# Kernel optimization log

Measured on AMD Instinct MI355X. Metric: run time of the kernel, lower is better.

Reference implementation:

```python
import jax, jax.numpy as jnp
import numpy as np

HEADS = 12
DIM = 768


def setup_inputs() -> dict:
    key = jax.random.key(0)
    ks = jax.random.split(key, 4)
    s = 0.02
    return {
        "x": jax.random.normal(ks[0], (8, 64, 64, DIM), dtype=jnp.float32),
        "w_qkv_h": jax.random.normal(ks[1], (DIM, 3 * DIM), dtype=jnp.float32) * s,
        "b_qkv_h": jnp.zeros((3 * DIM,), jnp.float32),
        "w_qkv_w": jax.random.normal(ks[2], (DIM, 3 * DIM), dtype=jnp.float32) * s,
        "b_qkv_w": jnp.zeros((3 * DIM,), jnp.float32),
        "w_proj": jax.random.normal(ks[3], (DIM, DIM), dtype=jnp.float32) * s,
        "b_proj": jnp.zeros((DIM,), jnp.float32),
    }


def _axial_attn(x_seq, w, b, heads, scale):
    # x_seq: [N, L, C]. Faithful to original torch code: q,k,v keep shape
    # [N, L, heads, hd]; matmul contracts hd, producing [N, L, heads, heads]
    # attention ACROSS HEADS at each position (no head permute in the source).
    N, L, C = x_seq.shape
    hd = C // heads
    qkv = (x_seq @ w + b).reshape(N, L, 3, heads, hd)
    q = qkv[:, :, 0] * scale
    k = qkv[:, :, 1]
    v = qkv[:, :, 2]
    attn = jax.nn.softmax(jnp.einsum('nlhd,nlgd->nlhg', q, k), axis=-1)
    out = jnp.einsum('nlhg,nlgd->nlhd', attn, v)
    return out.reshape(N, L, C)


def reference(x, w_qkv_h, b_qkv_h, w_qkv_w, b_qkv_w, w_proj, b_proj):
    B, H, W, C = x.shape
    scale = (C // HEADS) ** -0.5
    # H-axis pass: permute to [B, W, H, C], flatten batch*W
    x_h = jnp.transpose(x, (0, 2, 1, 3)).reshape(B * W, H, C)
    out_h = _axial_attn(x_h, w_qkv_h, b_qkv_h, HEADS, scale)
    out_h = jnp.transpose(out_h.reshape(B, W, H, C), (0, 2, 1, 3))
    # W-axis pass: flatten batch*H
    out_w = _axial_attn(x.reshape(B * H, W, C), w_qkv_w, b_qkv_w, HEADS, scale)
    out_w = out_w.reshape(B, H, W, C)
    # residual-style sum of the two axes, then output projection (dropout p=0)
    return (out_h + out_w) @ w_proj + b_proj
```

## Files before the change

kernel.cpp:

```cpp
#include <hip/hip_runtime.h>

typedef unsigned short u16;
typedef unsigned int u32;
typedef __attribute__((ext_vector_type(8))) short short8;
typedef __attribute__((ext_vector_type(4))) float f32x4;

#define DIMC 768
#define NQKV 2304
#define NPOS 32768
#define NKT 12

__device__ __forceinline__ float b2f(u16 u) {
    union { u32 i; float f; } c; c.i = ((u32)u) << 16; return c.f;
}
__device__ __forceinline__ u16 f2b(float f) {
    union { float f; u32 i; } c; c.f = f;
    u32 r = c.i + 0x7fffu + ((c.i >> 16) & 1u);
    return (u16)(r >> 16);
}

__device__ __forceinline__ void gl_lds16(const void* g, void* l) {
    __builtin_amdgcn_global_load_lds(
        (const __attribute__((address_space(1))) void*)g,
        (__attribute__((address_space(3))) void*)l, 16, 0, 0);
}

__global__ __launch_bounds__(256) void cvt_bf16(
    const float* __restrict__ in, u16* __restrict__ out, int n4)
{
    int i = blockIdx.x * 256 + threadIdx.x;
    if (i >= n4) return;
    float4 v = ((const float4*)in)[i];
    ushort4 o;
    o.x = f2b(v.x); o.y = f2b(v.y); o.z = f2b(v.z); o.w = f2b(v.w);
    ((ushort4*)out)[i] = o;
}

__global__ __launch_bounds__(256) void cvt_wT(
    const float* __restrict__ W0, const float* __restrict__ W1,
    const float* __restrict__ W2,
    u16* __restrict__ T0, u16* __restrict__ T1, u16* __restrict__ T2)
{
    const int z = blockIdx.z;
    const float* W = (z == 0) ? W0 : (z == 1) ? W1 : W2;
    u16* WT = (z == 0) ? T0 : (z == 1) ? T1 : T2;
    const int N = (z == 2) ? 768 : 2304;
    const int nb = blockIdx.x, kb = blockIdx.y;
    if (nb * 64 >= N) return;
    __shared__ u16 T[64][65];
    const int t = threadIdx.x, sr = t >> 2, sc = t & 3;
    {
        const float4* p = (const float4*)(W + (size_t)(kb * 64 + sr) * N + nb * 64 + sc * 16);
        float4 a0 = p[0], a1 = p[1], a2 = p[2], a3 = p[3];
        float vv[16] = {a0.x, a0.y, a0.z, a0.w, a1.x, a1.y, a1.z, a1.w,
                        a2.x, a2.y, a2.z, a2.w, a3.x, a3.y, a3.z, a3.w};
        #pragma unroll
        for (int i = 0; i < 16; ++i)
            T[sc * 16 + i][sr] = f2b(vv[i]);
    }
    __syncthreads();
    {
        u16 vv[16];
        #pragma unroll
        for (int i = 0; i < 16; ++i) vv[i] = T[sr][sc * 16 + i];
        uint4 p0, p1;
        p0.x = vv[0] | ((u32)vv[1] << 16);  p0.y = vv[2] | ((u32)vv[3] << 16);
        p0.z = vv[4] | ((u32)vv[5] << 16);  p0.w = vv[6] | ((u32)vv[7] << 16);
        p1.x = vv[8] | ((u32)vv[9] << 16);  p1.y = vv[10] | ((u32)vv[11] << 16);
        p1.z = vv[12] | ((u32)vv[13] << 16); p1.w = vv[14] | ((u32)vv[15] << 16);
        u16* q = WT + (size_t)(nb * 64 + sr) * DIMC + kb * 64 + sc * 16;
        *(uint4*)q = p0;
        *(uint4*)(q + 8) = p1;
    }
}


#define STAGE_A(buf, kt, ht) do {                                              \
    gl_lds16(aS + (size_t)((ht) * 128)      * DIMC + (size_t)(kt) * 64,        \
             &As[buf][(ht) * 8192 +        w * 512]);                          \
    gl_lds16(aS + (size_t)((ht) * 128 + 64) * DIMC + (size_t)(kt) * 64,        \
             &As[buf][(ht) * 8192 + 4096 + w * 512]);                          \
} while (0)

#define STAGE_B(buf, kt, ht) do {                                              \
    gl_lds16(bS + (size_t)((ht) * 128)      * DIMC + (size_t)(kt) * 64,        \
             &Bs[buf][(ht) * 8192 +        w * 512]);                          \
    gl_lds16(bS + (size_t)((ht) * 128 + 64) * DIMC + (size_t)(kt) * 64,        \
             &Bs[buf][(ht) * 8192 + 4096 + w * 512]);                          \
} while (0)

#define READ_A(base, hm) do {                                                  \
    _Pragma("unroll")                                                          \
    for (int i_ = 0; i_ < 4; ++i_) {                                           \
        const int row_ = (hm) * 128 + wm * 64 + i_ * 16 + lr;                  \
        _Pragma("unroll")                                                      \
        for (int ks_ = 0; ks_ < 2; ++ks_)                                      \
            af[i_][ks_] = *(const short8*)((base) + (row_ << 6) +              \
                              (((ks_ * 4 + lq) ^ (row_ & 7)) << 3));           \
    }                                                                          \
} while (0)

#define READ_B(dst, base, hn) do {                                             \
    _Pragma("unroll")                                                          \
    for (int j_ = 0; j_ < 2; ++j_) {                                           \
        const int row_ = (hn) * 128 + wn * 32 + j_ * 16 + lr;                  \
        _Pragma("unroll")                                                      \
        for (int ks_ = 0; ks_ < 2; ++ks_)                                      \
            (dst)[j_][ks_] = *(const short8*)((base) + (row_ << 6) +           \
                              (((ks_ * 4 + lq) ^ (row_ & 7)) << 3));           \
    }                                                                          \
} while (0)

#define MM(hm, hn, bsrc) do {                                                  \
    __builtin_amdgcn_s_setprio(1);                                             \
    _Pragma("unroll")                                                          \
    for (int i_ = 0; i_ < 4; ++i_)                                             \
        _Pragma("unroll")                                                      \
        for (int j_ = 0; j_ < 2; ++j_)                                         \
            _Pragma("unroll")                                                  \
            for (int ks_ = 0; ks_ < 2; ++ks_)                                  \
                acc[(hm) * 4 + i_][(hn) * 2 + j_] =                            \
                    __builtin_amdgcn_mfma_f32_16x16x32_bf16(                   \
                        af[i_][ks_], (bsrc)[j_][ks_],                          \
                        acc[(hm) * 4 + i_][(hn) * 2 + j_], 0, 0, 0);           \
    __builtin_amdgcn_s_setprio(0);                                             \
} while (0)

#define BAR() do {                                                             \
    __builtin_amdgcn_sched_barrier(0);                                         \
    __builtin_amdgcn_s_barrier();                                              \
    __builtin_amdgcn_sched_barrier(0);                                         \
} while (0)

#define KTILE(kt, S12, S34, VN) do {                                           \
    const int p_ = (kt) & 1, q_ = p_ ^ 1;                                      \
    const u16* Ab_ = As[p_];                                                   \
    const u16* Bb_ = Bs[p_];                                                   \
                                                             \
    READ_A(Ab_, 0);                                                            \
    READ_B(b0, Bb_, 0);                                                        \
    if (S12) STAGE_B(q_, (kt) + 1, 1);                                         \
    BAR();                                                                     \
    MM(0, 0, b0);                                                              \
                                                             \
    READ_B(b1, Bb_, 1);                                                        \
    if (S12) STAGE_A(q_, (kt) + 1, 1);                                         \
    BAR();                                                                     \
    MM(0, 1, b1);                                                              \
                                                             \
    READ_A(Ab_, 1);                                                            \
    if (S34) STAGE_A(p_, (kt) + 2, 0);                                         \
    BAR();                                                                     \
    MM(1, 0, b0);                                                              \
                                                             \
    if (S34) STAGE_B(p_, (kt) + 2, 0);                                         \
    __builtin_amdgcn_sched_barrier(0);                                         \
    asm volatile("s_waitcnt vmcnt(" VN ")" ::: "memory");                      \
    BAR();                                                                     \
    MM(1, 1, b1);                                                              \
} while (0)

__global__ __launch_bounds__(512, 2) void gemm256(
    const u16* __restrict__ A, const u16* __restrict__ BT,
    const float* __restrict__ bias, void* __restrict__ C,
    int ldn, int c_is_f32)
{
    __shared__ __align__(16) u16 As[2][256 * 64];
    __shared__ __align__(16) u16 Bs[2][256 * 64];

    const int t = threadIdx.x;
    const int w = t >> 6, l = t & 63;
    const int wm = w >> 2, wn = w & 3;
    const int lr = l & 15, lq = l >> 4;

    const int gx = (int)gridDim.x;
    const int nwg = gx * (int)gridDim.y;
    const int lin = (int)blockIdx.y * gx + (int)blockIdx.x;
    const int swz = (lin & 7) * (nwg >> 3) + (lin >> 3);
    const int by = swz / gx, bx = swz - by * gx;
    const int mBase = by * 256, nBase = bx * 256;

    const int srow = t >> 3;
    const int schk = (t & 7) ^ (srow & 7);
    const u16* aS = A  + (size_t)(mBase + srow) * DIMC + schk * 8;
    const u16* bS = BT + (size_t)(nBase + srow) * DIMC + schk * 8;

    f32x4 acc[8][4];
    #pragma unroll
    for (int i = 0; i < 8; ++i)
        #pragma unroll
        for (int j = 0; j < 4; ++j)
            acc[i][j] = (f32x4){0.f, 0.f, 0.f, 0.f};

    short8 af[4][2], b0[2][2], b1[2][2];

    STAGE_A(0, 0, 0); STAGE_B(0, 0, 0); STAGE_B(0, 0, 1); STAGE_A(0, 0, 1);
    STAGE_A(1, 1, 0); STAGE_B(1, 1, 0);
    __builtin_amdgcn_sched_barrier(0);
    asm volatile("s_waitcnt vmcnt(4)" ::: "memory");
    BAR();

    #pragma unroll 1
    for (int kt = 0; kt < NKT - 2; ++kt) { KTILE(kt, 1, 1, "4"); }
    { KTILE(NKT - 2, 1, 0, "0"); }
    { KTILE(NKT - 1, 0, 0, "0"); }

    #pragma unroll
    for (int hn = 0; hn < 2; ++hn)
        #pragma unroll
        for (int j = 0; j < 2; ++j) {
            const int col = nBase + hn * 128 + wn * 32 + j * 16 + lr;
            const float bb = bias[col];
            #pragma unroll
            for (int hm = 0; hm < 2; ++hm)
                #pragma unroll
                for (int i = 0; i < 4; ++i) {
                    const int row = mBase + hm * 128 + wm * 64 + i * 16 + lq * 4;
                    #pragma unroll
                    for (int rg = 0; rg < 4; ++rg) {
                        float v = acc[hm * 4 + i][hn * 2 + j][rg] + bb;
                        size_t idx = (size_t)(row + rg) * ldn + col;
                        if (c_is_f32) ((float*)C)[idx] = v;
                        else          ((u16*)C)[idx]   = f2b(v);
                    }
                }
        }
}

__device__ __forceinline__ void attn_one(
    short8 qa0, short8 qa1, short8 kb0, short8 kb1,
    const float* v, float* o, int lr)
{
    f32x4 s = (f32x4){0.f, 0.f, 0.f, 0.f};
    s = __builtin_amdgcn_mfma_f32_16x16x32_bf16(qa0, kb0, s, 0, 0, 0);
    s = __builtin_amdgcn_mfma_f32_16x16x32_bf16(qa1, kb1, s, 0, 0, 0);
    float pp[4];
    #pragma unroll
    for (int rg = 0; rg < 4; ++rg) {
        float x = (lr < 12) ? s[rg] * 0.125f : -1e30f;
        float m = x;
        m = fmaxf(m, __shfl_xor(m, 1));
        m = fmaxf(m, __shfl_xor(m, 2));
        m = fmaxf(m, __shfl_xor(m, 4));
        m = fmaxf(m, __shfl_xor(m, 8));
        float e = (lr < 12) ? __expf(x - m) : 0.f;
        float ss = e;
        ss += __shfl_xor(ss, 1);
        ss += __shfl_xor(ss, 2);
        ss += __shfl_xor(ss, 4);
        ss += __shfl_xor(ss, 8);
        pp[rg] = e / ss;
    }
    #pragma unroll
    for (int g = 0; g < 12; ++g) {
        #pragma unroll
        for (int h = 0; h < 12; ++h) {
            union { float f; int i; } cb;
            cb.i = __builtin_amdgcn_readlane(
                __builtin_bit_cast(int, pp[h & 3]), (h >> 2) * 16 + g);
            o[h] = fmaf(cb.f, v[g], o[h]);
        }
    }
}

__global__ __launch_bounds__(256) void headattn2(
    const u16* __restrict__ qkv1, const u16* __restrict__ qkv2,
    u16* __restrict__ sum)
{
    const int t = threadIdx.x, wv = t >> 6, l = t & 63;
    const int p = blockIdx.x * 4 + wv;
    const u16* r1 = qkv1 + (size_t)p * NQKV;
    const u16* r2 = qkv2 + (size_t)p * NQKV;
    const int lr = l & 15;
    const int fo = lr * 64 + (l >> 4) * 8;

    short8 qa0_1 = *(const short8*)(r1 + fo);
    short8 qa1_1 = *(const short8*)(r1 + fo + 32);
    short8 kb0_1 = *(const short8*)(r1 + 768 + fo);
    short8 kb1_1 = *(const short8*)(r1 + 768 + fo + 32);
    short8 qa0_2 = *(const short8*)(r2 + fo);
    short8 qa1_2 = *(const short8*)(r2 + fo + 32);
    short8 kb0_2 = *(const short8*)(r2 + 768 + fo);
    short8 kb1_2 = *(const short8*)(r2 + 768 + fo + 32);
    float v1[12], v2[12];
    #pragma unroll
    for (int g = 0; g < 12; ++g) {
        v1[g] = b2f(r1[1536 + g * 64 + l]);
        v2[g] = b2f(r2[1536 + g * 64 + l]);
    }

    float o[12];
    #pragma unroll
    for (int h = 0; h < 12; ++h) o[h] = 0.f;

    attn_one(qa0_1, qa1_1, kb0_1, kb1_1, v1, o, lr);
    attn_one(qa0_2, qa1_2, kb0_2, kb1_2, v2, o, lr);

    u16* orow = sum + (size_t)p * DIMC;
    #pragma unroll
    for (int h = 0; h < 12; ++h)
        orow[h * 64 + l] = f2b(o[h]);
}

extern "C" void kernel_launch(void* const* d_in, const int* in_sizes, int n_in,
                              void* d_out, int out_size, void* d_ws, size_t ws_size,
                              hipStream_t stream) {
    const float* x  = (const float*)d_in[0];
    const float* wh = (const float*)d_in[1];
    const float* bh = (const float*)d_in[2];
    const float* ww = (const float*)d_in[3];
    const float* bw = (const float*)d_in[4];
    const float* wp = (const float*)d_in[5];
    const float* bp = (const float*)d_in[6];
    float* out = (float*)d_out;

    u16* xb   = (u16*)d_ws;
    u16* sumb = xb;
    u16* whT  = xb   + 25165824;
    u16* wwT  = whT  + 1769472;
    u16* wpT  = wwT  + 1769472;
    u16* qkv1 = wpT  + 589824;
    u16* qkv2 = qkv1 + 75497472;

    cvt_bf16<<<24576, 256, 0, stream>>>(x, xb, 6291456);
    dim3 wg(36, 12, 3);
    cvt_wT<<<wg, 256, 0, stream>>>(wh, ww, wp, whT, wwT, wpT);

    dim3 gq(NQKV / 256, NPOS / 256);
    dim3 gp(DIMC / 256, NPOS / 256);

    gemm256<<<gq, 512, 0, stream>>>(xb, whT, bh, qkv1, NQKV, 0);
    gemm256<<<gq, 512, 0, stream>>>(xb, wwT, bw, qkv2, NQKV, 0);
    headattn2<<<NPOS / 4, 256, 0, stream>>>(qkv1, qkv2, sumb);
    gemm256<<<gp, 512, 0, stream>>>(sumb, wpT, bp, out, DIMC, 1);
}
```

Measured before the change: 617.8 us.

## Reorder GEMM k-loop staging and barriers with explicit lgkmcnt waits

Restructures the 256x256 bf16 GEMM main loop's software pipeline. Global-to-LDS stages are reassigned across the four MFMA phases so more of the next tile is prefetched earlier (an extra B half in the prologue, deeper vmcnt of 6). The sched_barrier-wrapped barriers are replaced by raw s_barrier plus explicit lgkmcnt waits, with a barrier after each MFMA block. The aim is better overlap of LDS reads, global loads and MFMA, at the cost of more barriers per tile and a risk of LDS hazards if the buffer reuse ordering is wrong.

```diff
diff --git a/kernel.cpp b/kernel.cpp
--- a/kernel.cpp
+++ b/kernel.cpp
@@ -126,38 +126,39 @@
     __builtin_amdgcn_s_setprio(0);                                             \
 } while (0)
 
-#define BAR() do {                                                             \
-    __builtin_amdgcn_sched_barrier(0);                                         \
-    __builtin_amdgcn_s_barrier();                                              \
-    __builtin_amdgcn_sched_barrier(0);                                         \
-} while (0)
-
-#define KTILE(kt, S12, S34, VN) do {                                           \
+#define KTILE(kt, S1, S2, S3, S4, VN) do {                                     \
     const int p_ = (kt) & 1, q_ = p_ ^ 1;                                      \
     const u16* Ab_ = As[p_];                                                   \
     const u16* Bb_ = Bs[p_];                                                   \
-                                                             \
+                                                 \
     READ_A(Ab_, 0);                                                            \
     READ_B(b0, Bb_, 0);                                                        \
-    if (S12) STAGE_B(q_, (kt) + 1, 1);                                         \
-    BAR();                                                                     \
+    if (S1) STAGE_A(q_, (kt) + 1, 1);                                          \
+    asm volatile("s_waitcnt lgkmcnt(8)" ::: "memory");                         \
+    __builtin_amdgcn_s_barrier();                                              \
+    asm volatile("s_waitcnt lgkmcnt(0)" ::: "memory");                         \
     MM(0, 0, b0);                                                              \
-                                                             \
+    __builtin_amdgcn_s_barrier();                                              \
+                                                 \
     READ_B(b1, Bb_, 1);                                                        \
-    if (S12) STAGE_A(q_, (kt) + 1, 1);                                         \
-    BAR();                                                                     \
+    if (S2) STAGE_A(p_, (kt) + 2, 0);                                          \
+    __builtin_amdgcn_s_barrier();                                              \
+    asm volatile("s_waitcnt lgkmcnt(0)" ::: "memory");                         \
     MM(0, 1, b1);                                                              \
-                                                             \
+    __builtin_amdgcn_s_barrier();                                              \
+                                                 \
     READ_A(Ab_, 1);                                                            \
-    if (S34) STAGE_A(p_, (kt) + 2, 0);                                         \
-    BAR();                                                                     \
+    if (S3) STAGE_B(p_, (kt) + 2, 0);                                          \
+    __builtin_amdgcn_s_barrier();                                              \
+    asm volatile("s_waitcnt lgkmcnt(0)" ::: "memory");                         \
     MM(1, 0, b0);                                                              \
-                                                             \
-    if (S34) STAGE_B(p_, (kt) + 2, 0);                                         \
-    __builtin_amdgcn_sched_barrier(0);                                         \
+    __builtin_amdgcn_s_barrier();                                              \
+                                                 \
+    if (S4) STAGE_B(p_, (kt) + 2, 1);                                          \
+    __builtin_amdgcn_s_barrier();                                              \
+    MM(1, 1, b1);                                                              \
     asm volatile("s_waitcnt vmcnt(" VN ")" ::: "memory");                      \
-    BAR();                                                                     \
-    MM(1, 1, b1);                                                              \
+    __builtin_amdgcn_s_barrier();                                              \
 } while (0)
 
 __global__ __launch_bounds__(512, 2) void gemm256(
@@ -195,15 +196,14 @@
     short8 af[4][2], b0[2][2], b1[2][2];
 
     STAGE_A(0, 0, 0); STAGE_B(0, 0, 0); STAGE_B(0, 0, 1); STAGE_A(0, 0, 1);
-    STAGE_A(1, 1, 0); STAGE_B(1, 1, 0);
-    __builtin_amdgcn_sched_barrier(0);
-    asm volatile("s_waitcnt vmcnt(4)" ::: "memory");
-    BAR();
+    STAGE_A(1, 1, 0); STAGE_B(1, 1, 0); STAGE_B(1, 1, 1);
+    asm volatile("s_waitcnt vmcnt(6)" ::: "memory");
+    __builtin_amdgcn_s_barrier();
 
     #pragma unroll 1
-    for (int kt = 0; kt < NKT - 2; ++kt) { KTILE(kt, 1, 1, "4"); }
-    { KTILE(NKT - 2, 1, 0, "0"); }
-    { KTILE(NKT - 1, 0, 0, "0"); }
+    for (int kt = 0; kt < NKT - 2; ++kt) { KTILE(kt, 1, 1, 1, 1, "6"); }
+    { KTILE(NKT - 2, 1, 0, 0, 0, "0"); }
+    { KTILE(NKT - 1, 0, 0, 0, 0, "0"); }
 
     #pragma unroll
     for (int hn = 0; hn < 2; ++hn)
```

After: 654.9 us. 1.06x slower.

## Merge both QKV GEMMs into one wide GEMM with direct-from-global B loads

Applied to the files above, without the earlier changes.

The two QKV projection GEMMs become a single GEMM over a concatenated weight (whT and wwT are adjacent in workspace) with N=4608, using a concatenated bias and an interleaved qkv output read by headattn2. Inside the GEMM, B fragments are now loaded straight from global memory into registers instead of through LDS. The freed LDS goes to triple-buffering A, and the block swizzle is changed to walk along N first. This removes one launch and the LDS traffic for B, at the cost of uncoalesced, unswizzled global B loads that sit on the MFMA critical path.

```diff
diff --git a/kernel.cpp b/kernel.cpp
--- a/kernel.cpp
+++ b/kernel.cpp
@@ -6,7 +6,6 @@
 typedef __attribute__((ext_vector_type(4))) float f32x4;
 
 #define DIMC 768
-#define NQKV 2304
 #define NPOS 32768
 #define NKT 12
 
@@ -74,19 +73,21 @@
     }
 }
 
+__global__ __launch_bounds__(256) void biascat(
+    const float* __restrict__ bh, const float* __restrict__ bw,
+    float* __restrict__ o)
+{
+    int i = blockIdx.x * 256 + threadIdx.x;
+    if (i < 2304) o[i] = bh[i];
+    else if (i < 4608) o[i] = bw[i - 2304];
+}
+
 
 #define STAGE_A(buf, kt, ht) do {                                              \
     gl_lds16(aS + (size_t)((ht) * 128)      * DIMC + (size_t)(kt) * 64,        \
              &As[buf][(ht) * 8192 +        w * 512]);                          \
     gl_lds16(aS + (size_t)((ht) * 128 + 64) * DIMC + (size_t)(kt) * 64,        \
              &As[buf][(ht) * 8192 + 4096 + w * 512]);                          \
-} while (0)
-
-#define STAGE_B(buf, kt, ht) do {                                              \
-    gl_lds16(bS + (size_t)((ht) * 128)      * DIMC + (size_t)(kt) * 64,        \
-             &Bs[buf][(ht) * 8192 +        w * 512]);                          \
-    gl_lds16(bS + (size_t)((ht) * 128 + 64) * DIMC + (size_t)(kt) * 64,        \
-             &Bs[buf][(ht) * 8192 + 4096 + w * 512]);                          \
 } while (0)
 
 #define READ_A(base, hm) do {                                                  \
@@ -100,14 +101,14 @@
     }                                                                          \
 } while (0)
 
-#define READ_B(dst, base, hn) do {                                             \
+#define GLOAD_B(dst, kt, hn) do {                                              \
     _Pragma("unroll")                                                          \
     for (int j_ = 0; j_ < 2; ++j_) {                                           \
-        const int row_ = (hn) * 128 + wn * 32 + j_ * 16 + lr;                  \
+        const int row_ = nBase + (hn) * 128 + wn * 32 + j_ * 16 + lr;          \
         _Pragma("unroll")                                                      \
         for (int ks_ = 0; ks_ < 2; ++ks_)                                      \
-            (dst)[j_][ks_] = *(const short8*)((base) + (row_ << 6) +           \
-                              (((ks_ * 4 + lq) ^ (row_ & 7)) << 3));           \
+            (dst)[j_][ks_] = *(const short8*)(BT + (size_t)row_ * DIMC +       \
+                              (size_t)(kt) * 64 + (ks_ * 4 + lq) * 8);         \
     }                                                                          \
 } while (0)
 
@@ -132,28 +133,24 @@
     __builtin_amdgcn_sched_barrier(0);                                         \
 } while (0)
 
-#define KTILE(kt, S12, S34, VN) do {                                           \
-    const int p_ = (kt) & 1, q_ = p_ ^ 1;                                      \
-    const u16* Ab_ = As[p_];                                                   \
-    const u16* Bb_ = Bs[p_];                                                   \
+#define KTILE(kt, S34, VN) do {                                                \
+    const int p_ = (kt) % 3, s_ = ((kt) + 2) % 3;                              \
                                                              \
-    READ_A(Ab_, 0);                                                            \
-    READ_B(b0, Bb_, 0);                                                        \
-    if (S12) STAGE_B(q_, (kt) + 1, 1);                                         \
+    READ_A(As[p_], 0);                                                         \
+    GLOAD_B(b0, kt, 0);                                                        \
+    GLOAD_B(b1, kt, 1);                                                        \
     BAR();                                                                     \
     MM(0, 0, b0);                                                              \
                                                              \
-    READ_B(b1, Bb_, 1);                                                        \
-    if (S12) STAGE_A(q_, (kt) + 1, 1);                                         \
     BAR();                                                                     \
     MM(0, 1, b1);                                                              \
                                                              \
-    READ_A(Ab_, 1);                                                            \
-    if (S34) STAGE_A(p_, (kt) + 2, 0);                                         \
+    READ_A(As[p_], 1);                                                         \
+    if (S34) STAGE_A(s_, (kt) + 2, 0);                                         \
     BAR();                                                                     \
     MM(1, 0, b0);                                                              \
                                                              \
-    if (S34) STAGE_B(p_, (kt) + 2, 0);                                         \
+    if (S34) STAGE_A(s_, (kt) + 2, 1);                                         \
     __builtin_amdgcn_sched_barrier(0);                                         \
     asm volatile("s_waitcnt vmcnt(" VN ")" ::: "memory");                      \
     BAR();                                                                     \
@@ -165,25 +162,23 @@
     const float* __restrict__ bias, void* __restrict__ C,
     int ldn, int c_is_f32)
 {
-    __shared__ __align__(16) u16 As[2][256 * 64];
-    __shared__ __align__(16) u16 Bs[2][256 * 64];
+    __shared__ __align__(16) u16 As[3][256 * 64];
 
     const int t = threadIdx.x;
     const int w = t >> 6, l = t & 63;
     const int wm = w >> 2, wn = w & 3;
     const int lr = l & 15, lq = l >> 4;
 
-    const int gx = (int)gridDim.x;
-    const int nwg = gx * (int)gridDim.y;
+    const int gx = (int)gridDim.x, gy = (int)gridDim.y;
+    const int nwg = gx * gy;
     const int lin = (int)blockIdx.y * gx + (int)blockIdx.x;
     const int swz = (lin & 7) * (nwg >> 3) + (lin >> 3);
-    const int by = swz / gx, bx = swz - by * gx;
+    const int bx = swz / gy, by = swz - bx * gy;
     const int mBase = by * 256, nBase = bx * 256;
 
     const int srow = t >> 3;
     const int schk = (t & 7) ^ (srow & 7);
-    const u16* aS = A  + (size_t)(mBase + srow) * DIMC + schk * 8;
-    const u16* bS = BT + (size_t)(nBase + srow) * DIMC + schk * 8;
+    const u16* aS = A + (size_t)(mBase + srow) * DIMC + schk * 8;
 
     f32x4 acc[8][4];
     #pragma unroll
@@ -194,16 +189,16 @@
 
     short8 af[4][2], b0[2][2], b1[2][2];
 
-    STAGE_A(0, 0, 0); STAGE_B(0, 0, 0); STAGE_B(0, 0, 1); STAGE_A(0, 0, 1);
-    STAGE_A(1, 1, 0); STAGE_B(1, 1, 0);
+    STAGE_A(0, 0, 0); STAGE_A(0, 0, 1);
+    STAGE_A(1, 1, 0); STAGE_A(1, 1, 1);
     __builtin_amdgcn_sched_barrier(0);
     asm volatile("s_waitcnt vmcnt(4)" ::: "memory");
     BAR();
 
     #pragma unroll 1
-    for (int kt = 0; kt < NKT - 2; ++kt) { KTILE(kt, 1, 1, "4"); }
-    { KTILE(NKT - 2, 1, 0, "0"); }
-    { KTILE(NKT - 1, 0, 0, "0"); }
+    for (int kt = 0; kt < NKT - 2; ++kt) { KTILE(kt, 1, "4"); }
+    { KTILE(NKT - 2, 0, "0"); }
+    { KTILE(NKT - 1, 0, "0"); }
 
     #pragma unroll
     for (int hn = 0; hn < 2; ++hn)
@@ -264,13 +259,12 @@
 }
 
 __global__ __launch_bounds__(256) void headattn2(
-    const u16* __restrict__ qkv1, const u16* __restrict__ qkv2,
-    u16* __restrict__ sum)
+    const u16* __restrict__ qkv, u16* __restrict__ sum)
 {
     const int t = threadIdx.x, wv = t >> 6, l = t & 63;
     const int p = blockIdx.x * 4 + wv;
-    const u16* r1 = qkv1 + (size_t)p * NQKV;
-    const u16* r2 = qkv2 + (size_t)p * NQKV;
+    const u16* r1 = qkv + (size_t)p * 4608;
+    const u16* r2 = r1 + 2304;
     const int lr = l & 15;
     const int fo = lr * 64 + (l >> 4) * 8;
 
@@ -319,18 +313,18 @@
     u16* whT  = xb   + 25165824;
     u16* wwT  = whT  + 1769472;
     u16* wpT  = wwT  + 1769472;
-    u16* qkv1 = wpT  + 589824;
-    u16* qkv2 = qkv1 + 75497472;
+    float* bcat = (float*)(wpT + 589824);
+    u16* qkvc = wpT + 589824 + 9216;
 
     cvt_bf16<<<24576, 256, 0, stream>>>(x, xb, 6291456);
     dim3 wg(36, 12, 3);
     cvt_wT<<<wg, 256, 0, stream>>>(wh, ww, wp, whT, wwT, wpT);
-
-    dim3 gq(NQKV / 256, NPOS / 256);
+    biascat<<<18, 256, 0, stream>>>(bh, bw, bcat);
+
+    dim3 gq(4608 / 256, NPOS / 256);
     dim3 gp(DIMC / 256, NPOS / 256);
 
-    gemm256<<<gq, 512, 0, stream>>>(xb, whT, bh, qkv1, NQKV, 0);
-    gemm256<<<gq, 512, 0, stream>>>(xb, wwT, bw, qkv2, NQKV, 0);
-    headattn2<<<NPOS / 4, 256, 0, stream>>>(qkv1, qkv2, sumb);
+    gemm256<<<gq, 512, 0, stream>>>(xb, whT, bcat, qkvc, 4608, 0);
+    headattn2<<<NPOS / 4, 256, 0, stream>>>(qkvc, sumb);
     gemm256<<<gp, 512, 0, stream>>>(sumb, wpT, bp, out, DIMC, 1);
 }
```

Result: slower. 789.6 us (+27.8%).
